# Performance work log

Measured on AMD Instinct MI355X. Metric: run time of the kernel, lower is better.

Reference implementation:

```python
import jax, jax.numpy as jnp
import numpy as np


def setup_inputs() -> dict:
    key = jax.random.key(0)
    ks = jax.random.split(key, 10)
    B, T, E = 4096, 200, 64
    H0, H1, H2 = 80, 40, 1
    D = 4 * E  # concat feature dim = 256
    glorot = lambda k, shp: jax.random.normal(k, shp, jnp.float32) * jnp.sqrt(2.0 / (shp[0] + shp[1]))
    return {
        "queries": jax.random.normal(ks[0], (B, 1, E), jnp.float32),
        "keys": jax.random.normal(ks[1], (B, T, E), jnp.float32),
        "keys_length": jax.random.randint(ks[2], (B, 1), 0, T, jnp.int32),
        "W0": glorot(ks[3], (D, H0)),
        "b0": jnp.zeros((H0,), jnp.float32),
        "W1": glorot(ks[4], (H0, H1)),
        "b1": jnp.zeros((H1,), jnp.float32),
        "W2": glorot(ks[5], (H1, H2)),
        "b2": jnp.zeros((H2,), jnp.float32),
    }


def reference(queries, keys, keys_length, W0, b0, W1, b1, W2, b2):
    B, T, E = keys.shape
    # repeat query along history axis: [B,1,E] -> [B,T,E]
    q = jnp.broadcast_to(queries, (B, T, E))
    # DIN attention input: [B,T,4E]
    att = jnp.concatenate([q, keys, q - keys, q * keys], axis=-1)
    # tiny 3-layer MLP, sigmoid activations (att_activation, no output_activation override)
    h = jax.nn.sigmoid(att @ W0 + b0)
    h = jax.nn.sigmoid(h @ W1 + b1)
    score = jax.nn.sigmoid(h @ W2 + b2)          # [B,T,1]
    out = jnp.transpose(score, (0, 2, 1))         # [B,1,T]
    # sequence mask: [B,1,T]
    key_masks = jnp.arange(T)[None, None, :] < keys_length[:, :, None]
    # weight_normalization=False -> masked positions become 0, no softmax
    out = jnp.where(key_masks, out, jnp.zeros_like(out))
    # weighted sum over history: [B,1,T] @ [B,T,E] -> [B,1,E]
    return jnp.matmul(out, keys)
```

## Files before the change

### kernel.cpp

```cpp
#include <hip/hip_runtime.h>

#define NT 512
#define NWAVE 8
#define PE 136
#define PW1 88
#define PH 88
#define UPB 7
#define BPC 64
#define SPC (BPC * UPB)

typedef __attribute__((ext_vector_type(8))) short short8;
typedef __attribute__((ext_vector_type(4))) float f32x4;

__device__ __forceinline__ unsigned short f2b(float f) {
  unsigned int x = __float_as_uint(f);
  return (unsigned short)((x + 0x7fffu + ((x >> 16) & 1u)) >> 16);
}
__device__ __forceinline__ float sigmoidf(float x) {
  return __builtin_amdgcn_rcpf(1.0f + __expf(-x));
}
__device__ __forceinline__ short8 pack8(float4 a, float4 b) {
  short8 r;
  r[0] = (short)f2b(a.x); r[1] = (short)f2b(a.y); r[2] = (short)f2b(a.z); r[3] = (short)f2b(a.w);
  r[4] = (short)f2b(b.x); r[5] = (short)f2b(b.y); r[6] = (short)f2b(b.z); r[7] = (short)f2b(b.w);
  return r;
}
__device__ __forceinline__ short8 pack8q(float4 a, float4 b, float4 qa, float4 qb) {
  short8 r;
  r[0] = (short)f2b(a.x * qa.x); r[1] = (short)f2b(a.y * qa.y);
  r[2] = (short)f2b(a.z * qa.z); r[3] = (short)f2b(a.w * qa.w);
  r[4] = (short)f2b(b.x * qb.x); r[5] = (short)f2b(b.y * qb.y);
  r[6] = (short)f2b(b.z * qb.z); r[7] = (short)f2b(b.w * qb.w);
  return r;
}

__global__ __launch_bounds__(256, 2) void prep_c(
    const float* __restrict__ q, const float* __restrict__ W0,
    const float* __restrict__ b0, float* __restrict__ C, int B)
{
  __shared__ float Wac[64 * 80];
  __shared__ float qlds[32 * 64];
  const int bbase = blockIdx.x * 32, tid = threadIdx.x;
  for (int idx = tid; idx < 5120; idx += 256) {
    const int e = idx / 80, h = idx - e * 80;
    Wac[idx] = W0[e * 80 + h] + W0[(128 + e) * 80 + h];
  }
  for (int idx = tid; idx < 2048; idx += 256) {
    const int bl = idx >> 6, e = idx & 63;
    const int bg = bbase + bl;
    qlds[idx] = (bg < B) ? q[bg * 64 + e] : 0.0f;
  }
  __syncthreads();
  #pragma unroll
  for (int i = 0; i < 10; ++i) {
    const int idx = tid + i * 256;
    const int bl = idx / 80, h = idx - bl * 80;
    const int bg = bbase + bl;
    if (bg < B) {
      float acc = b0[h];
      #pragma unroll 8
      for (int e = 0; e < 64; ++e) acc += qlds[bl * 64 + e] * Wac[e * 80 + h];
      C[bg * 80 + h] = acc;
    }
  }
}

__global__ __launch_bounds__(NT, 2) void din_attn_main(
    const float* __restrict__ q,
    const float* __restrict__ keys,
    const int* __restrict__ klen,
    const float* __restrict__ W0,
    const float* __restrict__ b0,
    const float* __restrict__ W1,
    const float* __restrict__ b1,
    const float* __restrict__ W2,
    const float* __restrict__ b2,
    float* __restrict__ out,
    const float* __restrict__ Cpre,
    unsigned int* __restrict__ ctrs,
    int B)
{
  __shared__ __align__(16) unsigned short WxT[80 * PE];
  __shared__ __align__(16) unsigned short W1T[48 * PW1];
  __shared__ __align__(16) unsigned short h0s[NWAVE][32 * PH];
  __shared__ __align__(16) float scb[NWAVE][32];

  const int tid = threadIdx.x;

  for (int idx = tid; idx < 128 * 80; idx += NT) {
    const int e = idx / 80, h = idx - e * 80;
    const float v = (e < 64)
        ? (W0[(64 + e) * 80 + h] - W0[(128 + e) * 80 + h])
        : W0[(128 + e) * 80 + h];
    WxT[h * PE + e] = f2b(v);
  }
  for (int idx = tid; idx < 48 * PW1; idx += NT) {
    const int j = idx / PW1, h = idx - j * PW1;
    W1T[idx] = (j < 40 && h < 80) ? f2b(W1[h * 40 + j]) : (unsigned short)0;
  }
  __syncthreads();

  const int wv = __builtin_amdgcn_readfirstlane(tid >> 6);
  const int lane = tid & 63;
  const int lm = lane & 15;
  const int quad = lane >> 4;
  const int gw = blockIdx.x * NWAVE + wv;
  unsigned short* h0 = h0s[wv];
  float* scl = scb[wv];

  float b1v[3], w2v[3];
  #pragma unroll
  for (int nt = 0; nt < 3; ++nt) {
    const int col = nt * 16 + lm;
    b1v[nt] = (col < 40) ? b1[col] : 0.0f;
    w2v[nt] = (col < 40) ? W2[col] : 0.0f;
  }
  const float b2v = b2[0];
  const short8 z8 = {0, 0, 0, 0, 0, 0, 0, 0};
  const float4 z4 = {0.0f, 0.0f, 0.0f, 0.0f};

  auto unit = [&](int b, int u, int L) {
    const float4* q4 = (const float4*)(q + (size_t)b * 64);
    const float4 q0 = q4[quad * 2],     q1 = q4[quad * 2 + 1];
    const float4 q2 = q4[8 + quad * 2], q3 = q4[8 + quad * 2 + 1];

    float cfv[5];
    if (Cpre != nullptr) {
      #pragma unroll
      for (int nt = 0; nt < 5; ++nt) cfv[nt] = Cpre[b * 80 + nt * 16 + lm];
    } else {
      #pragma unroll
      for (int nt = 0; nt < 5; ++nt) cfv[nt] = b0[nt * 16 + lm];
      for (int e = 0; e < 64; ++e) {
        const float qv = q[(size_t)b * 64 + e];
        #pragma unroll
        for (int nt = 0; nt < 5; ++nt)
          cfv[nt] += qv * (W0[e * 80 + nt * 16 + lm] + W0[(128 + e) * 80 + nt * 16 + lm]);
      }
    }

    const float* kb = keys + (size_t)b * 12800;
    const int t0 = u << 5;
    const int nr = min(32, L - t0);
    const bool two = nr > 16;

    short8 a0, a1, aq0, aq1;
    {
      const int t = t0 + lm;
      float4 k0 = z4, k1 = z4, k2 = z4, k3 = z4;
      if (t < L) {
        const float4* kp = (const float4*)(kb + (size_t)t * 64);
        k0 = kp[quad * 2]; k1 = kp[quad * 2 + 1];
        k2 = kp[8 + quad * 2]; k3 = kp[8 + quad * 2 + 1];
      }
      a0 = pack8(k0, k1); a1 = pack8(k2, k3);
      aq0 = pack8q(k0, k1, q0, q1); aq1 = pack8q(k2, k3, q2, q3);
    }
    short8 c0 = z8, c1 = z8, cq0 = z8, cq1 = z8;
    if (two) {
      const int t = t0 + 16 + lm;
      float4 k0 = z4, k1 = z4, k2 = z4, k3 = z4;
      if (t < L) {
        const float4* kp = (const float4*)(kb + (size_t)t * 64);
        k0 = kp[quad * 2]; k1 = kp[quad * 2 + 1];
        k2 = kp[8 + quad * 2]; k3 = kp[8 + quad * 2 + 1];
      }
      c0 = pack8(k0, k1); c1 = pack8(k2, k3);
      cq0 = pack8q(k0, k1, q0, q1); cq1 = pack8q(k2, k3, q2, q3);
    }

    #pragma unroll
    for (int nt = 0; nt < 5; ++nt) {
      const int col = nt * 16 + lm;
      const unsigned short* wr = &WxT[col * PE + quad * 8];
      const short8 w0 = *(const short8*)(wr);
      const short8 w1 = *(const short8*)(wr + 32);
      const short8 w2 = *(const short8*)(wr + 64);
      const short8 w3 = *(const short8*)(wr + 96);
      f32x4 acc;
      acc[0] = cfv[nt]; acc[1] = cfv[nt]; acc[2] = cfv[nt]; acc[3] = cfv[nt];
      acc = __builtin_amdgcn_mfma_f32_16x16x32_bf16(a0,  w0, acc, 0, 0, 0);
      acc = __builtin_amdgcn_mfma_f32_16x16x32_bf16(a1,  w1, acc, 0, 0, 0);
      acc = __builtin_amdgcn_mfma_f32_16x16x32_bf16(aq0, w2, acc, 0, 0, 0);
      acc = __builtin_amdgcn_mfma_f32_16x16x32_bf16(aq1, w3, acc, 0, 0, 0);
      #pragma unroll
      for (int r = 0; r < 4; ++r)
        h0[(quad * 4 + r) * PH + col] = f2b(sigmoidf(acc[r]));
      if (two) {
        f32x4 ac2;
        ac2[0] = cfv[nt]; ac2[1] = cfv[nt]; ac2[2] = cfv[nt]; ac2[3] = cfv[nt];
        ac2 = __builtin_amdgcn_mfma_f32_16x16x32_bf16(c0,  w0, ac2, 0, 0, 0);
        ac2 = __builtin_amdgcn_mfma_f32_16x16x32_bf16(c1,  w1, ac2, 0, 0, 0);
        ac2 = __builtin_amdgcn_mfma_f32_16x16x32_bf16(cq0, w2, ac2, 0, 0, 0);
        ac2 = __builtin_amdgcn_mfma_f32_16x16x32_bf16(cq1, w3, ac2, 0, 0, 0);
        #pragma unroll
        for (int r = 0; r < 4; ++r)
          h0[(16 + quad * 4 + r) * PH + col] = f2b(sigmoidf(ac2[r]));
      }
    }

    const short8 ha00 = *(const short8*)&h0[lm * PH + quad * 8];
    const short8 ha01 = *(const short8*)&h0[lm * PH + 32 + quad * 8];
    short8 ha02 = z8;
    if (quad < 2) ha02 = *(const short8*)&h0[lm * PH + 64 + quad * 8];
    short8 ha10 = z8, ha11 = z8, ha12 = z8;
    if (two) {
      ha10 = *(const short8*)&h0[(16 + lm) * PH + quad * 8];
      ha11 = *(const short8*)&h0[(16 + lm) * PH + 32 + quad * 8];
      if (quad < 2) ha12 = *(const short8*)&h0[(16 + lm) * PH + 64 + quad * 8];
    }
    float pd0[4] = {0, 0, 0, 0}, pd1[4] = {0, 0, 0, 0};
    #pragma unroll
    for (int nt = 0; nt < 3; ++nt) {
      const int col = nt * 16 + lm;
      const unsigned short* wr = &W1T[col * PW1 + quad * 8];
      const short8 wb0 = *(const short8*)(wr);
      const short8 wb1 = *(const short8*)(wr + 32);
      short8 wb2 = z8;
      if (quad < 2) wb2 = *(const short8*)(wr + 64);
      f32x4 acc;
      acc[0] = b1v[nt]; acc[1] = b1v[nt]; acc[2] = b1v[nt]; acc[3] = b1v[nt];
      acc = __builtin_amdgcn_mfma_f32_16x16x32_bf16(ha00, wb0, acc, 0, 0, 0);
      acc = __builtin_amdgcn_mfma_f32_16x16x32_bf16(ha01, wb1, acc, 0, 0, 0);
      acc = __builtin_amdgcn_mfma_f32_16x16x32_bf16(ha02, wb2, acc, 0, 0, 0);
      #pragma unroll
      for (int r = 0; r < 4; ++r) pd0[r] += sigmoidf(acc[r]) * w2v[nt];
      if (two) {
        f32x4 ac2;
        ac2[0] = b1v[nt]; ac2[1] = b1v[nt]; ac2[2] = b1v[nt]; ac2[3] = b1v[nt];
        ac2 = __builtin_amdgcn_mfma_f32_16x16x32_bf16(ha10, wb0, ac2, 0, 0, 0);
        ac2 = __builtin_amdgcn_mfma_f32_16x16x32_bf16(ha11, wb1, ac2, 0, 0, 0);
        ac2 = __builtin_amdgcn_mfma_f32_16x16x32_bf16(ha12, wb2, ac2, 0, 0, 0);
        #pragma unroll
        for (int r = 0; r < 4; ++r) pd1[r] += sigmoidf(ac2[r]) * w2v[nt];
      }
    }
    #pragma unroll
    for (int r = 0; r < 4; ++r) {
      pd0[r] += __shfl_xor(pd0[r], 1);
      pd0[r] += __shfl_xor(pd0[r], 2);
      pd0[r] += __shfl_xor(pd0[r], 4);
      pd0[r] += __shfl_xor(pd0[r], 8);
    }
    if (two) {
      #pragma unroll
      for (int r = 0; r < 4; ++r) {
        pd1[r] += __shfl_xor(pd1[r], 1);
        pd1[r] += __shfl_xor(pd1[r], 2);
        pd1[r] += __shfl_xor(pd1[r], 4);
        pd1[r] += __shfl_xor(pd1[r], 8);
      }
    }
    if (lm == 0) {
      #pragma unroll
      for (int r = 0; r < 4; ++r) scl[quad * 4 + r] = sigmoidf(pd0[r] + b2v);
      if (two) {
        #pragma unroll
        for (int r = 0; r < 4; ++r) scl[16 + quad * 4 + r] = sigmoidf(pd1[r] + b2v);
      }
    }
    float4 sv[8];
    #pragma unroll
    for (int i = 0; i < 8; ++i) sv[i] = *(const float4*)&scl[i * 4];

    const float* kcol = kb + (size_t)t0 * 64 + lane;
    float wacc = 0.0f;
    #pragma unroll
    for (int t = 0; t < 32; ++t) {
      if (t < nr) {
        const int i = t >> 2, j = t & 3;
        const float s = (j == 0) ? sv[i].x : (j == 1) ? sv[i].y : (j == 2) ? sv[i].z : sv[i].w;
        wacc += s * kcol[(size_t)t * 64];
      }
    }
    atomicAdd(&out[(size_t)b * 64 + lane], wacc);
  };

  if (ctrs != nullptr) {
    const int c = gw >> 6;
    unsigned int* ctr = ctrs + (size_t)c * 32;
    unsigned int v0 = 0u;
    if (lane == 0) v0 = atomicAdd(ctr, 1u);
    int s = (int)__builtin_amdgcn_readfirstlane(v0);
    while (s < SPC) {
      unsigned int vn = 0u;
      if (lane == 0) vn = atomicAdd(ctr, 1u);
      const int b = (c << 6) + (s & 63);
      const int u = s >> 6;
      if (b < B) {
        int L = klen[b];
        L = __builtin_amdgcn_readfirstlane(max(0, min(200, L)));
        if (u * 32 < L) unit(b, u, L);
      }
      s = (int)__builtin_amdgcn_readfirstlane(vn);
    }
  } else {
    const int b = gw;
    if (b < B) {
      int L = klen[b];
      L = __builtin_amdgcn_readfirstlane(max(0, min(200, L)));
      for (int u = 0; u * 32 < L; ++u) unit(b, u, L);
    }
  }
}

extern "C" void kernel_launch(void* const* d_in, const int* in_sizes, int n_in,
                              void* d_out, int out_size, void* d_ws, size_t ws_size,
                              hipStream_t stream) {
  const int B = in_sizes[2];
  const size_t csize = (size_t)B * 80 * sizeof(float);
  const int nctr = (B + BPC - 1) / BPC;
  const size_t ctrbytes = (size_t)nctr * 32 * sizeof(unsigned int);

  const float* Cpre = nullptr;
  unsigned int* ctrs = nullptr;
  size_t off = 0;
  if (ws_size >= csize) { Cpre = (const float*)d_ws; off = csize; }
  off = (off + 127) & ~(size_t)127;
  if (ws_size >= off + ctrbytes) {
    ctrs = (unsigned int*)((char*)d_ws + off);
    hipMemsetAsync(ctrs, 0, ctrbytes, stream);
  }
  hipMemsetAsync(d_out, 0, (size_t)out_size, stream);

  if (Cpre != nullptr) {
    prep_c<<<(B + 31) / 32, 256, 0, stream>>>(
        (const float*)d_in[0], (const float*)d_in[3], (const float*)d_in[4],
        (float*)d_ws, B);
  }
  din_attn_main<<<(B + NWAVE - 1) / NWAVE, NT, 0, stream>>>(
      (const float*)d_in[0], (const float*)d_in[1], (const int*)d_in[2],
      (const float*)d_in[3], (const float*)d_in[4], (const float*)d_in[5],
      (const float*)d_in[6], (const float*)d_in[7], (const float*)d_in[8],
      (float*)d_out, Cpre, ctrs, B);
}
```

Before: 370.7 us.

## Build compact work list, software-prefetch next unit, and vectorize weighted-sum reduction

A new pre-kernel builds a compact global list of only the valid (batch, chunk) units, so the main kernel no longer pops masked-out slots from per-cluster counters. The main loop is restructured to prefetch the next unit's keys, klen and C values while computing the current one, hiding global latency. The final weighted sum now uses float4 loads with cross-quad shuffles and fewer atomics instead of going through shared memory. This costs an extra kernel launch, global atomics while building the list, and higher register pressure from the prefetch state.

```diff
diff --git a/kernel.cpp b/kernel.cpp
--- a/kernel.cpp
+++ b/kernel.cpp
@@ -6,8 +6,6 @@
 #define PW1 88
 #define PH 88
 #define UPB 7
-#define BPC 64
-#define SPC (BPC * UPB)
 
 typedef __attribute__((ext_vector_type(8))) short short8;
 typedef __attribute__((ext_vector_type(4))) float f32x4;
@@ -61,6 +59,21 @@
       #pragma unroll 8
       for (int e = 0; e < 64; ++e) acc += qlds[bl * 64 + e] * Wac[e * 80 + h];
       C[bg * 80 + h] = acc;
+    }
+  }
+}
+
+__global__ void build_wl(const int* __restrict__ klen, unsigned* __restrict__ hdr,
+                         unsigned* __restrict__ wl, int B)
+{
+  const int b = blockIdx.x * 256 + threadIdx.x;
+  if (b < B) {
+    int L = klen[b];
+    L = max(0, min(200, L));
+    const int nu = (L + 31) >> 5;
+    for (int u = 0; u < nu; ++u) {
+      const unsigned pos = atomicAdd(&hdr[0], 1u);
+      wl[pos] = ((unsigned)u << 16) | (unsigned)b;
     }
   }
 }
@@ -77,13 +90,13 @@
     const float* __restrict__ b2,
     float* __restrict__ out,
     const float* __restrict__ Cpre,
-    unsigned int* __restrict__ ctrs,
+    unsigned* __restrict__ hdr,
+    const unsigned* __restrict__ wl,
     int B)
 {
   __shared__ __align__(16) unsigned short WxT[80 * PE];
   __shared__ __align__(16) unsigned short W1T[48 * PW1];
   __shared__ __align__(16) unsigned short h0s[NWAVE][32 * PH];
-  __shared__ __align__(16) float scb[NWAVE][32];
 
   const int tid = threadIdx.x;
 
@@ -106,7 +119,8 @@
   const int quad = lane >> 4;
   const int gw = blockIdx.x * NWAVE + wv;
   unsigned short* h0 = h0s[wv];
-  float* scl = scb[wv];
+  const bool dyn = (hdr != nullptr);
+  unsigned* pop = dyn ? (hdr + 32) : nullptr;
 
   float b1v[3], w2v[3];
   #pragma unroll
@@ -117,68 +131,106 @@
   }
   const float b2v = b2[0];
   const short8 z8 = {0, 0, 0, 0, 0, 0, 0, 0};
-  const float4 z4 = {0.0f, 0.0f, 0.0f, 0.0f};
-
-  auto unit = [&](int b, int u, int L) {
-    const float4* q4 = (const float4*)(q + (size_t)b * 64);
-    const float4 q0 = q4[quad * 2],     q1 = q4[quad * 2 + 1];
-    const float4 q2 = q4[8 + quad * 2], q3 = q4[8 + quad * 2 + 1];
-
-    float cfv[5];
+
+  auto pf = [&](int s, int& pb, int& pu, int& pL,
+                float4& K0, float4& K1, float4& K2, float4& K3,
+                float& C0, float& C1, float& C2, float& C3, float& C4) {
+    int b, u;
+    if (dyn) { const unsigned e = wl[s]; b = (int)(e & 0xFFFFu); u = (int)(e >> 16); }
+    else     { b = gw; u = s - gw * UPB; }
+    pb = b; pu = u;
+    pL = klen[b];
     if (Cpre != nullptr) {
-      #pragma unroll
-      for (int nt = 0; nt < 5; ++nt) cfv[nt] = Cpre[b * 80 + nt * 16 + lm];
+      const float* cp = Cpre + (size_t)b * 80 + lm;
+      C0 = cp[0]; C1 = cp[16]; C2 = cp[32]; C3 = cp[48]; C4 = cp[64];
     } else {
-      #pragma unroll
-      for (int nt = 0; nt < 5; ++nt) cfv[nt] = b0[nt * 16 + lm];
+      C0 = b0[lm]; C1 = b0[16 + lm]; C2 = b0[32 + lm]; C3 = b0[48 + lm]; C4 = b0[64 + lm];
       for (int e = 0; e < 64; ++e) {
         const float qv = q[(size_t)b * 64 + e];
-        #pragma unroll
-        for (int nt = 0; nt < 5; ++nt)
-          cfv[nt] += qv * (W0[e * 80 + nt * 16 + lm] + W0[(128 + e) * 80 + nt * 16 + lm]);
-      }
-    }
-
-    const float* kb = keys + (size_t)b * 12800;
-    const int t0 = u << 5;
-    const int nr = min(32, L - t0);
-    const bool two = nr > 16;
-
-    short8 a0, a1, aq0, aq1;
-    {
-      const int t = t0 + lm;
-      float4 k0 = z4, k1 = z4, k2 = z4, k3 = z4;
-      if (t < L) {
-        const float4* kp = (const float4*)(kb + (size_t)t * 64);
-        k0 = kp[quad * 2]; k1 = kp[quad * 2 + 1];
-        k2 = kp[8 + quad * 2]; k3 = kp[8 + quad * 2 + 1];
-      }
-      a0 = pack8(k0, k1); a1 = pack8(k2, k3);
-      aq0 = pack8q(k0, k1, q0, q1); aq1 = pack8q(k2, k3, q2, q3);
-    }
+        C0 += qv * (W0[e * 80 + lm] + W0[(128 + e) * 80 + lm]);
+        C1 += qv * (W0[e * 80 + 16 + lm] + W0[(128 + e) * 80 + 16 + lm]);
+        C2 += qv * (W0[e * 80 + 32 + lm] + W0[(128 + e) * 80 + 32 + lm]);
+        C3 += qv * (W0[e * 80 + 48 + lm] + W0[(128 + e) * 80 + 48 + lm]);
+        C4 += qv * (W0[e * 80 + 64 + lm] + W0[(128 + e) * 80 + 64 + lm]);
+      }
+    }
+    const int t = min(u * 32 + lm, 199);
+    const float4* kp = (const float4*)(keys + (size_t)b * 12800 + (size_t)t * 64);
+    K0 = kp[quad * 2]; K1 = kp[quad * 2 + 1];
+    K2 = kp[8 + quad * 2]; K3 = kp[8 + quad * 2 + 1];
+  };
+
+  int s, nwl;
+  if (dyn) {
+    unsigned v0 = 0u;
+    if (lane == 0) v0 = atomicAdd(pop, 1u);
+    s = (int)__builtin_amdgcn_readfirstlane((int)v0);
+    nwl = (int)__builtin_amdgcn_readfirstlane((int)hdr[0]);
+  } else {
+    s = gw * UPB;
+    nwl = (gw < B) ? (gw * UPB + UPB) : s;
+  }
+
+  int cb = 0, cu = 0, cL = 0;
+  float4 ck0, ck1, ck2, ck3;
+  float cc0 = 0, cc1 = 0, cc2 = 0, cc3 = 0, cc4 = 0;
+  if (s < nwl) pf(s, cb, cu, cL, ck0, ck1, ck2, ck3, cc0, cc1, cc2, cc3, cc4);
+  unsigned vp = 0u;
+  if (dyn && lane == 0) vp = atomicAdd(pop, 1u);
+
+  while (s < nwl) {
+    const float4* q4p = (const float4*)(q + (size_t)cb * 64);
+    const float4 q0 = q4p[quad * 2], q1 = q4p[quad * 2 + 1];
+    const float4 q2v = q4p[8 + quad * 2], q3v = q4p[8 + quad * 2 + 1];
+
+    const int Ls = max(0, min(200, __builtin_amdgcn_readfirstlane(cL)));
+    const int t0 = cu << 5;
+
+    const bool v0ok = (t0 + lm) < Ls;
+    short8 a0 = pack8(ck0, ck1), a1 = pack8(ck2, ck3);
+    short8 aq0 = pack8q(ck0, ck1, q0, q1), aq1 = pack8q(ck2, ck3, q2v, q3v);
+    if (!v0ok) { a0 = z8; a1 = z8; aq0 = z8; aq1 = z8; }
+
+    int s2;
+    if (dyn) {
+      s2 = (int)__builtin_amdgcn_readfirstlane((int)vp);
+      if (lane == 0) vp = atomicAdd(pop, 1u);
+    } else {
+      s2 = s + 1;
+    }
+
+    const bool twoS = (Ls - t0) > 16;
+    float4 e0, e1, e2, e3;
+    if (twoS) {
+      const int t1 = min(t0 + 16 + lm, 199);
+      const float4* kp = (const float4*)(keys + (size_t)cb * 12800 + (size_t)t1 * 64);
+      e0 = kp[quad * 2]; e1 = kp[quad * 2 + 1];
+      e2 = kp[8 + quad * 2]; e3 = kp[8 + quad * 2 + 1];
+    }
+    int nb = 0, nu_ = 0, nL = 0;
+    float4 nk0, nk1, nk2, nk3;
+    float nc0 = 0, nc1 = 0, nc2 = 0, nc3 = 0, nc4 = 0;
+    if (s2 < nwl) pf(s2, nb, nu_, nL, nk0, nk1, nk2, nk3, nc0, nc1, nc2, nc3, nc4);
+
     short8 c0 = z8, c1 = z8, cq0 = z8, cq1 = z8;
-    if (two) {
-      const int t = t0 + 16 + lm;
-      float4 k0 = z4, k1 = z4, k2 = z4, k3 = z4;
-      if (t < L) {
-        const float4* kp = (const float4*)(kb + (size_t)t * 64);
-        k0 = kp[quad * 2]; k1 = kp[quad * 2 + 1];
-        k2 = kp[8 + quad * 2]; k3 = kp[8 + quad * 2 + 1];
-      }
-      c0 = pack8(k0, k1); c1 = pack8(k2, k3);
-      cq0 = pack8q(k0, k1, q0, q1); cq1 = pack8q(k2, k3, q2, q3);
+    if (twoS) {
+      const bool v1ok = (t0 + 16 + lm) < Ls;
+      c0 = pack8(e0, e1); c1 = pack8(e2, e3);
+      cq0 = pack8q(e0, e1, q0, q1); cq1 = pack8q(e2, e3, q2v, q3v);
+      if (!v1ok) { c0 = z8; c1 = z8; cq0 = z8; cq1 = z8; }
     }
 
     #pragma unroll
     for (int nt = 0; nt < 5; ++nt) {
       const int col = nt * 16 + lm;
+      const float cv = (nt == 0) ? cc0 : (nt == 1) ? cc1 : (nt == 2) ? cc2 : (nt == 3) ? cc3 : cc4;
       const unsigned short* wr = &WxT[col * PE + quad * 8];
       const short8 w0 = *(const short8*)(wr);
       const short8 w1 = *(const short8*)(wr + 32);
       const short8 w2 = *(const short8*)(wr + 64);
       const short8 w3 = *(const short8*)(wr + 96);
       f32x4 acc;
-      acc[0] = cfv[nt]; acc[1] = cfv[nt]; acc[2] = cfv[nt]; acc[3] = cfv[nt];
+      acc[0] = cv; acc[1] = cv; acc[2] = cv; acc[3] = cv;
       acc = __builtin_amdgcn_mfma_f32_16x16x32_bf16(a0,  w0, acc, 0, 0, 0);
       acc = __builtin_amdgcn_mfma_f32_16x16x32_bf16(a1,  w1, acc, 0, 0, 0);
       acc = __builtin_amdgcn_mfma_f32_16x16x32_bf16(aq0, w2, acc, 0, 0, 0);
@@ -186,9 +238,9 @@
       #pragma unroll
       for (int r = 0; r < 4; ++r)
         h0[(quad * 4 + r) * PH + col] = f2b(sigmoidf(acc[r]));
-      if (two) {
+      if (twoS) {
         f32x4 ac2;
-        ac2[0] = cfv[nt]; ac2[1] = cfv[nt]; ac2[2] = cfv[nt]; ac2[3] = cfv[nt];
+        ac2[0] = cv; ac2[1] = cv; ac2[2] = cv; ac2[3] = cv;
         ac2 = __builtin_amdgcn_mfma_f32_16x16x32_bf16(c0,  w0, ac2, 0, 0, 0);
         ac2 = __builtin_amdgcn_mfma_f32_16x16x32_bf16(c1,  w1, ac2, 0, 0, 0);
         ac2 = __builtin_amdgcn_mfma_f32_16x16x32_bf16(cq0, w2, ac2, 0, 0, 0);
@@ -204,7 +256,7 @@
     short8 ha02 = z8;
     if (quad < 2) ha02 = *(const short8*)&h0[lm * PH + 64 + quad * 8];
     short8 ha10 = z8, ha11 = z8, ha12 = z8;
-    if (two) {
+    if (twoS) {
       ha10 = *(const short8*)&h0[(16 + lm) * PH + quad * 8];
       ha11 = *(const short8*)&h0[(16 + lm) * PH + 32 + quad * 8];
       if (quad < 2) ha12 = *(const short8*)&h0[(16 + lm) * PH + 64 + quad * 8];
@@ -225,7 +277,7 @@
       acc = __builtin_amdgcn_mfma_f32_16x16x32_bf16(ha02, wb2, acc, 0, 0, 0);
       #pragma unroll
       for (int r = 0; r < 4; ++r) pd0[r] += sigmoidf(acc[r]) * w2v[nt];
-      if (two) {
+      if (twoS) {
         f32x4 ac2;
         ac2[0] = b1v[nt]; ac2[1] = b1v[nt]; ac2[2] = b1v[nt]; ac2[3] = b1v[nt];
         ac2 = __builtin_amdgcn_mfma_f32_16x16x32_bf16(ha10, wb0, ac2, 0, 0, 0);
@@ -242,7 +294,7 @@
       pd0[r] += __shfl_xor(pd0[r], 4);
       pd0[r] += __shfl_xor(pd0[r], 8);
     }
-    if (two) {
+    if (twoS) {
       #pragma unroll
       for (int r = 0; r < 4; ++r) {
         pd1[r] += __shfl_xor(pd1[r], 1);
@@ -251,56 +303,42 @@
         pd1[r] += __shfl_xor(pd1[r], 8);
       }
     }
-    if (lm == 0) {
-      #pragma unroll
-      for (int r = 0; r < 4; ++r) scl[quad * 4 + r] = sigmoidf(pd0[r] + b2v);
-      if (two) {
-        #pragma unroll
-        for (int r = 0; r < 4; ++r) scl[16 + quad * 4 + r] = sigmoidf(pd1[r] + b2v);
-      }
-    }
-    float4 sv[8];
-    #pragma unroll
-    for (int i = 0; i < 8; ++i) sv[i] = *(const float4*)&scl[i * 4];
-
-    const float* kcol = kb + (size_t)t0 * 64 + lane;
-    float wacc = 0.0f;
-    #pragma unroll
-    for (int t = 0; t < 32; ++t) {
-      if (t < nr) {
-        const int i = t >> 2, j = t & 3;
-        const float s = (j == 0) ? sv[i].x : (j == 1) ? sv[i].y : (j == 2) ? sv[i].z : sv[i].w;
-        wacc += s * kcol[(size_t)t * 64];
-      }
-    }
-    atomicAdd(&out[(size_t)b * 64 + lane], wacc);
-  };
-
-  if (ctrs != nullptr) {
-    const int c = gw >> 6;
-    unsigned int* ctr = ctrs + (size_t)c * 32;
-    unsigned int v0 = 0u;
-    if (lane == 0) v0 = atomicAdd(ctr, 1u);
-    int s = (int)__builtin_amdgcn_readfirstlane(v0);
-    while (s < SPC) {
-      unsigned int vn = 0u;
-      if (lane == 0) vn = atomicAdd(ctr, 1u);
-      const int b = (c << 6) + (s & 63);
-      const int u = s >> 6;
-      if (b < B) {
-        int L = klen[b];
-        L = __builtin_amdgcn_readfirstlane(max(0, min(200, L)));
-        if (u * 32 < L) unit(b, u, L);
-      }
-      s = (int)__builtin_amdgcn_readfirstlane(vn);
-    }
-  } else {
-    const int b = gw;
-    if (b < B) {
-      int L = klen[b];
-      L = __builtin_amdgcn_readfirstlane(max(0, min(200, L)));
-      for (int u = 0; u * 32 < L; ++u) unit(b, u, L);
-    }
+    float sc0[4], sc1[4];
+    #pragma unroll
+    for (int r = 0; r < 4; ++r) {
+      const int ta = t0 + 4 * quad + r;
+      sc0[r] = (ta < Ls) ? sigmoidf(pd0[r] + b2v) : 0.0f;
+      sc1[r] = (twoS && (ta + 16) < Ls) ? sigmoidf(pd1[r] + b2v) : 0.0f;
+    }
+
+    const float* kb = keys + (size_t)cb * 12800;
+    float4 w4 = {0.0f, 0.0f, 0.0f, 0.0f};
+    #pragma unroll
+    for (int r = 0; r < 4; ++r) {
+      const int ta = t0 + 4 * quad + r;
+      const float4 kva = *(const float4*)(kb + (size_t)min(ta, 199) * 64 + 4 * lm);
+      w4.x += sc0[r] * kva.x; w4.y += sc0[r] * kva.y;
+      w4.z += sc0[r] * kva.z; w4.w += sc0[r] * kva.w;
+      if (twoS) {
+        const float4 kvb = *(const float4*)(kb + (size_t)min(ta + 16, 199) * 64 + 4 * lm);
+        w4.x += sc1[r] * kvb.x; w4.y += sc1[r] * kvb.y;
+        w4.z += sc1[r] * kvb.z; w4.w += sc1[r] * kvb.w;
+      }
+    }
+    w4.x += __shfl_xor(w4.x, 16); w4.y += __shfl_xor(w4.y, 16);
+    w4.z += __shfl_xor(w4.z, 16); w4.w += __shfl_xor(w4.w, 16);
+    w4.x += __shfl_xor(w4.x, 32); w4.y += __shfl_xor(w4.y, 32);
+    w4.z += __shfl_xor(w4.z, 32); w4.w += __shfl_xor(w4.w, 32);
+    if (lane < 16) {
+      float* op = out + (size_t)cb * 64 + 4 * lm;
+      atomicAdd(op + 0, w4.x); atomicAdd(op + 1, w4.y);
+      atomicAdd(op + 2, w4.z); atomicAdd(op + 3, w4.w);
+    }
+
+    cb = nb; cu = nu_; cL = nL;
+    ck0 = nk0; ck1 = nk1; ck2 = nk2; ck3 = nk3;
+    cc0 = nc0; cc1 = nc1; cc2 = nc2; cc3 = nc3; cc4 = nc4;
+    s = s2;
   }
 }
 
@@ -309,20 +347,25 @@
                               hipStream_t stream) {
   const int B = in_sizes[2];
   const size_t csize = (size_t)B * 80 * sizeof(float);
-  const int nctr = (B + BPC - 1) / BPC;
-  const size_t ctrbytes = (size_t)nctr * 32 * sizeof(unsigned int);
+  const size_t wlbytes = (size_t)B * UPB * sizeof(unsigned);
 
   const float* Cpre = nullptr;
-  unsigned int* ctrs = nullptr;
+  unsigned* hdr = nullptr;
+  unsigned* wl = nullptr;
   size_t off = 0;
   if (ws_size >= csize) { Cpre = (const float*)d_ws; off = csize; }
   off = (off + 127) & ~(size_t)127;
-  if (ws_size >= off + ctrbytes) {
-    ctrs = (unsigned int*)((char*)d_ws + off);
-    hipMemsetAsync(ctrs, 0, ctrbytes, stream);
+  if (ws_size >= off + 256 + wlbytes) {
+    hdr = (unsigned*)((char*)d_ws + off);
+    wl = hdr + 64;
+    hipMemsetAsync(hdr, 0, 256, stream);
   }
   hipMemsetAsync(d_out, 0, (size_t)out_size, stream);
 
+  if (hdr != nullptr) {
+    build_wl<<<(B + 255) / 256, 256, 0, stream>>>(
+        (const int*)d_in[2], hdr, wl, B);
+  }
   if (Cpre != nullptr) {
     prep_c<<<(B + 31) / 32, 256, 0, stream>>>(
         (const float*)d_in[0], (const float*)d_in[3], (const float*)d_in[4],
@@ -332,5 +375,5 @@
       (const float*)d_in[0], (const float*)d_in[1], (const int*)d_in[2],
       (const float*)d_in[3], (const float*)d_in[4], (const float*)d_in[5],
       (const float*)d_in[6], (const float*)d_in[7], (const float*)d_in[8],
-      (float*)d_out, Cpre, ctrs, B);
-}
+      (float*)d_out, Cpre, hdr, (const unsigned*)wl, B);
+}
```

Result: slower. 544.2 us (+46.8%).

## Replace atomic work-stealing with one-wave-per-batch loop and prefetched keys

Applied to the files above, without the earlier changes.

Drops the per-chunk atomic counter scheduler and the atomicAdd accumulation. Each wave now owns one batch row and loops over its 32-step chunks, prefetching the next chunk's keys while computing the current one. The weighted sum is kept in registers and reduced with shuffles into a single float4 store, which also removes both memsets. It adds s_setprio around the MFMA sections. The trade-off is the loss of dynamic load balancing: keys_length varies from 0 to 199, so waves with long rows become stragglers.

```diff
diff --git a/kernel.cpp b/kernel.cpp
--- a/kernel.cpp
+++ b/kernel.cpp
@@ -5,9 +5,6 @@
 #define PE 136
 #define PW1 88
 #define PH 88
-#define UPB 7
-#define BPC 64
-#define SPC (BPC * UPB)
 
 typedef __attribute__((ext_vector_type(8))) short short8;
 typedef __attribute__((ext_vector_type(4))) float f32x4;
@@ -77,13 +74,11 @@
     const float* __restrict__ b2,
     float* __restrict__ out,
     const float* __restrict__ Cpre,
-    unsigned int* __restrict__ ctrs,
     int B)
 {
   __shared__ __align__(16) unsigned short WxT[80 * PE];
   __shared__ __align__(16) unsigned short W1T[48 * PW1];
   __shared__ __align__(16) unsigned short h0s[NWAVE][32 * PH];
-  __shared__ __align__(16) float scb[NWAVE][32];
 
   const int tid = threadIdx.x;
 
@@ -104,25 +99,18 @@
   const int lane = tid & 63;
   const int lm = lane & 15;
   const int quad = lane >> 4;
-  const int gw = blockIdx.x * NWAVE + wv;
+  const int b = blockIdx.x * NWAVE + wv;
   unsigned short* h0 = h0s[wv];
-  float* scl = scb[wv];
-
-  float b1v[3], w2v[3];
-  #pragma unroll
-  for (int nt = 0; nt < 3; ++nt) {
-    const int col = nt * 16 + lm;
-    b1v[nt] = (col < 40) ? b1[col] : 0.0f;
-    w2v[nt] = (col < 40) ? W2[col] : 0.0f;
-  }
-  const float b2v = b2[0];
   const short8 z8 = {0, 0, 0, 0, 0, 0, 0, 0};
-  const float4 z4 = {0.0f, 0.0f, 0.0f, 0.0f};
-
-  auto unit = [&](int b, int u, int L) {
-    const float4* q4 = (const float4*)(q + (size_t)b * 64);
-    const float4 q0 = q4[quad * 2],     q1 = q4[quad * 2 + 1];
-    const float4 q2 = q4[8 + quad * 2], q3 = q4[8 + quad * 2 + 1];
+
+  if (b < B) {
+    int L = klen[b];
+    L = __builtin_amdgcn_readfirstlane(max(0, min(200, L)));
+    const int nu = (L + 31) >> 5;
+
+    const float4* q4p = (const float4*)(q + (size_t)b * 64);
+    const float4 q0 = q4p[quad * 2], q1 = q4p[quad * 2 + 1];
+    const float4 q2 = q4p[8 + quad * 2], q3 = q4p[8 + quad * 2 + 1];
 
     float cfv[5];
     if (Cpre != nullptr) {
@@ -138,169 +126,167 @@
           cfv[nt] += qv * (W0[e * 80 + nt * 16 + lm] + W0[(128 + e) * 80 + nt * 16 + lm]);
       }
     }
-
-    const float* kb = keys + (size_t)b * 12800;
-    const int t0 = u << 5;
-    const int nr = min(32, L - t0);
-    const bool two = nr > 16;
-
-    short8 a0, a1, aq0, aq1;
-    {
-      const int t = t0 + lm;
-      float4 k0 = z4, k1 = z4, k2 = z4, k3 = z4;
-      if (t < L) {
-        const float4* kp = (const float4*)(kb + (size_t)t * 64);
-        k0 = kp[quad * 2]; k1 = kp[quad * 2 + 1];
-        k2 = kp[8 + quad * 2]; k3 = kp[8 + quad * 2 + 1];
-      }
-      a0 = pack8(k0, k1); a1 = pack8(k2, k3);
-      aq0 = pack8q(k0, k1, q0, q1); aq1 = pack8q(k2, k3, q2, q3);
-    }
-    short8 c0 = z8, c1 = z8, cq0 = z8, cq1 = z8;
-    if (two) {
-      const int t = t0 + 16 + lm;
-      float4 k0 = z4, k1 = z4, k2 = z4, k3 = z4;
-      if (t < L) {
-        const float4* kp = (const float4*)(kb + (size_t)t * 64);
-        k0 = kp[quad * 2]; k1 = kp[quad * 2 + 1];
-        k2 = kp[8 + quad * 2]; k3 = kp[8 + quad * 2 + 1];
-      }
-      c0 = pack8(k0, k1); c1 = pack8(k2, k3);
-      cq0 = pack8q(k0, k1, q0, q1); cq1 = pack8q(k2, k3, q2, q3);
-    }
-
-    #pragma unroll
-    for (int nt = 0; nt < 5; ++nt) {
-      const int col = nt * 16 + lm;
-      const unsigned short* wr = &WxT[col * PE + quad * 8];
-      const short8 w0 = *(const short8*)(wr);
-      const short8 w1 = *(const short8*)(wr + 32);
-      const short8 w2 = *(const short8*)(wr + 64);
-      const short8 w3 = *(const short8*)(wr + 96);
-      f32x4 acc;
-      acc[0] = cfv[nt]; acc[1] = cfv[nt]; acc[2] = cfv[nt]; acc[3] = cfv[nt];
-      acc = __builtin_amdgcn_mfma_f32_16x16x32_bf16(a0,  w0, acc, 0, 0, 0);
-      acc = __builtin_amdgcn_mfma_f32_16x16x32_bf16(a1,  w1, acc, 0, 0, 0);
-      acc = __builtin_amdgcn_mfma_f32_16x16x32_bf16(aq0, w2, acc, 0, 0, 0);
-      acc = __builtin_amdgcn_mfma_f32_16x16x32_bf16(aq1, w3, acc, 0, 0, 0);
-      #pragma unroll
-      for (int r = 0; r < 4; ++r)
-        h0[(quad * 4 + r) * PH + col] = f2b(sigmoidf(acc[r]));
-      if (two) {
-        f32x4 ac2;
-        ac2[0] = cfv[nt]; ac2[1] = cfv[nt]; ac2[2] = cfv[nt]; ac2[3] = cfv[nt];
-        ac2 = __builtin_amdgcn_mfma_f32_16x16x32_bf16(c0,  w0, ac2, 0, 0, 0);
-        ac2 = __builtin_amdgcn_mfma_f32_16x16x32_bf16(c1,  w1, ac2, 0, 0, 0);
-        ac2 = __builtin_amdgcn_mfma_f32_16x16x32_bf16(cq0, w2, ac2, 0, 0, 0);
-        ac2 = __builtin_amdgcn_mfma_f32_16x16x32_bf16(cq1, w3, ac2, 0, 0, 0);
-        #pragma unroll
-        for (int r = 0; r < 4; ++r)
-          h0[(16 + quad * 4 + r) * PH + col] = f2b(sigmoidf(ac2[r]));
-      }
-    }
-
-    const short8 ha00 = *(const short8*)&h0[lm * PH + quad * 8];
-    const short8 ha01 = *(const short8*)&h0[lm * PH + 32 + quad * 8];
-    short8 ha02 = z8;
-    if (quad < 2) ha02 = *(const short8*)&h0[lm * PH + 64 + quad * 8];
-    short8 ha10 = z8, ha11 = z8, ha12 = z8;
-    if (two) {
-      ha10 = *(const short8*)&h0[(16 + lm) * PH + quad * 8];
-      ha11 = *(const short8*)&h0[(16 + lm) * PH + 32 + quad * 8];
-      if (quad < 2) ha12 = *(const short8*)&h0[(16 + lm) * PH + 64 + quad * 8];
-    }
-    float pd0[4] = {0, 0, 0, 0}, pd1[4] = {0, 0, 0, 0};
+    float b1v[3], w2v[3];
     #pragma unroll
     for (int nt = 0; nt < 3; ++nt) {
       const int col = nt * 16 + lm;
-      const unsigned short* wr = &W1T[col * PW1 + quad * 8];
-      const short8 wb0 = *(const short8*)(wr);
-      const short8 wb1 = *(const short8*)(wr + 32);
-      short8 wb2 = z8;
-      if (quad < 2) wb2 = *(const short8*)(wr + 64);
-      f32x4 acc;
-      acc[0] = b1v[nt]; acc[1] = b1v[nt]; acc[2] = b1v[nt]; acc[3] = b1v[nt];
-      acc = __builtin_amdgcn_mfma_f32_16x16x32_bf16(ha00, wb0, acc, 0, 0, 0);
-      acc = __builtin_amdgcn_mfma_f32_16x16x32_bf16(ha01, wb1, acc, 0, 0, 0);
-      acc = __builtin_amdgcn_mfma_f32_16x16x32_bf16(ha02, wb2, acc, 0, 0, 0);
-      #pragma unroll
-      for (int r = 0; r < 4; ++r) pd0[r] += sigmoidf(acc[r]) * w2v[nt];
-      if (two) {
-        f32x4 ac2;
-        ac2[0] = b1v[nt]; ac2[1] = b1v[nt]; ac2[2] = b1v[nt]; ac2[3] = b1v[nt];
-        ac2 = __builtin_amdgcn_mfma_f32_16x16x32_bf16(ha10, wb0, ac2, 0, 0, 0);
-        ac2 = __builtin_amdgcn_mfma_f32_16x16x32_bf16(ha11, wb1, ac2, 0, 0, 0);
-        ac2 = __builtin_amdgcn_mfma_f32_16x16x32_bf16(ha12, wb2, ac2, 0, 0, 0);
+      b1v[nt] = (col < 40) ? b1[col] : 0.0f;
+      w2v[nt] = (col < 40) ? W2[col] : 0.0f;
+    }
+    const float b2v = b2[0];
+
+    const float* kb = keys + (size_t)b * 12800;
+    float4 w4 = {0.0f, 0.0f, 0.0f, 0.0f};
+
+    float4 pk0, pk1, pk2, pk3;
+    if (nu > 0) {
+      const float4* kp = (const float4*)(kb + (size_t)min(lm, 199) * 64);
+      pk0 = kp[quad * 2]; pk1 = kp[quad * 2 + 1];
+      pk2 = kp[8 + quad * 2]; pk3 = kp[8 + quad * 2 + 1];
+    }
+
+    for (int u = 0; u < nu; ++u) {
+      const int t0 = u << 5;
+      const bool twoS = (L - t0) > 16;
+
+      short8 a0 = pack8(pk0, pk1), a1 = pack8(pk2, pk3);
+      short8 aq0 = pack8q(pk0, pk1, q0, q1), aq1 = pack8q(pk2, pk3, q2, q3);
+      if (!((t0 + lm) < L)) { a0 = z8; a1 = z8; aq0 = z8; aq1 = z8; }
+
+      float4 e0, e1, e2, e3;
+      if (twoS) {
+        const float4* kp = (const float4*)(kb + (size_t)min(t0 + 16 + lm, 199) * 64);
+        e0 = kp[quad * 2]; e1 = kp[quad * 2 + 1];
+        e2 = kp[8 + quad * 2]; e3 = kp[8 + quad * 2 + 1];
+      }
+      if (u + 1 < nu) {
+        const float4* kp = (const float4*)(kb + (size_t)min(t0 + 32 + lm, 199) * 64);
+        pk0 = kp[quad * 2]; pk1 = kp[quad * 2 + 1];
+        pk2 = kp[8 + quad * 2]; pk3 = kp[8 + quad * 2 + 1];
+      }
+
+      short8 c0 = z8, c1 = z8, cq0 = z8, cq1 = z8;
+      if (twoS) {
+        c0 = pack8(e0, e1); c1 = pack8(e2, e3);
+        cq0 = pack8q(e0, e1, q0, q1); cq1 = pack8q(e2, e3, q2, q3);
+        if (!((t0 + 16 + lm) < L)) { c0 = z8; c1 = z8; cq0 = z8; cq1 = z8; }
+      }
+
+      __builtin_amdgcn_s_setprio(1);
+      #pragma unroll
+      for (int nt = 0; nt < 5; ++nt) {
+        const int col = nt * 16 + lm;
+        const unsigned short* wr = &WxT[col * PE + quad * 8];
+        const short8 w0 = *(const short8*)(wr);
+        const short8 w1 = *(const short8*)(wr + 32);
+        const short8 w2 = *(const short8*)(wr + 64);
+        const short8 w3 = *(const short8*)(wr + 96);
+        f32x4 acc;
+        acc[0] = cfv[nt]; acc[1] = cfv[nt]; acc[2] = cfv[nt]; acc[3] = cfv[nt];
+        acc = __builtin_amdgcn_mfma_f32_16x16x32_bf16(a0,  w0, acc, 0, 0, 0);
+        acc = __builtin_amdgcn_mfma_f32_16x16x32_bf16(a1,  w1, acc, 0, 0, 0);
+        acc = __builtin_amdgcn_mfma_f32_16x16x32_bf16(aq0, w2, acc, 0, 0, 0);
+        acc = __builtin_amdgcn_mfma_f32_16x16x32_bf16(aq1, w3, acc, 0, 0, 0);
         #pragma unroll
-        for (int r = 0; r < 4; ++r) pd1[r] += sigmoidf(ac2[r]) * w2v[nt];
-      }
-    }
-    #pragma unroll
-    for (int r = 0; r < 4; ++r) {
-      pd0[r] += __shfl_xor(pd0[r], 1);
-      pd0[r] += __shfl_xor(pd0[r], 2);
-      pd0[r] += __shfl_xor(pd0[r], 4);
-      pd0[r] += __shfl_xor(pd0[r], 8);
-    }
-    if (two) {
+        for (int r = 0; r < 4; ++r)
+          h0[(quad * 4 + r) * PH + col] = f2b(sigmoidf(acc[r]));
+        if (twoS) {
+          f32x4 ac2;
+          ac2[0] = cfv[nt]; ac2[1] = cfv[nt]; ac2[2] = cfv[nt]; ac2[3] = cfv[nt];
+          ac2 = __builtin_amdgcn_mfma_f32_16x16x32_bf16(c0,  w0, ac2, 0, 0, 0);
+          ac2 = __builtin_amdgcn_mfma_f32_16x16x32_bf16(c1,  w1, ac2, 0, 0, 0);
+          ac2 = __builtin_amdgcn_mfma_f32_16x16x32_bf16(cq0, w2, ac2, 0, 0, 0);
+          ac2 = __builtin_amdgcn_mfma_f32_16x16x32_bf16(cq1, w3, ac2, 0, 0, 0);
+          #pragma unroll
+          for (int r = 0; r < 4; ++r)
+            h0[(16 + quad * 4 + r) * PH + col] = f2b(sigmoidf(ac2[r]));
+        }
+      }
+      __builtin_amdgcn_s_setprio(0);
+
+      const short8 ha00 = *(const short8*)&h0[lm * PH + quad * 8];
+      const short8 ha01 = *(const short8*)&h0[lm * PH + 32 + quad * 8];
+      short8 ha02 = z8;
+      if (quad < 2) ha02 = *(const short8*)&h0[lm * PH + 64 + quad * 8];
+      short8 ha10 = z8, ha11 = z8, ha12 = z8;
+      if (twoS) {
+        ha10 = *(const short8*)&h0[(16 + lm) * PH + quad * 8];
+        ha11 = *(const short8*)&h0[(16 + lm) * PH + 32 + quad * 8];
+        if (quad < 2) ha12 = *(const short8*)&h0[(16 + lm) * PH + 64 + quad * 8];
+      }
+      float pd0[4] = {0, 0, 0, 0}, pd1[4] = {0, 0, 0, 0};
+      __builtin_amdgcn_s_setprio(1);
+      #pragma unroll
+      for (int nt = 0; nt < 3; ++nt) {
+        const int col = nt * 16 + lm;
+        const unsigned short* wr = &W1T[col * PW1 + quad * 8];
+        const short8 wb0 = *(const short8*)(wr);
+        const short8 wb1 = *(const short8*)(wr + 32);
+        short8 wb2 = z8;
+        if (quad < 2) wb2 = *(const short8*)(wr + 64);
+        f32x4 acc;
+        acc[0] = b1v[nt]; acc[1] = b1v[nt]; acc[2] = b1v[nt]; acc[3] = b1v[nt];
+        acc = __builtin_amdgcn_mfma_f32_16x16x32_bf16(ha00, wb0, acc, 0, 0, 0);
+        acc = __builtin_amdgcn_mfma_f32_16x16x32_bf16(ha01, wb1, acc, 0, 0, 0);
+        acc = __builtin_amdgcn_mfma_f32_16x16x32_bf16(ha02, wb2, acc, 0, 0, 0);
+        #pragma unroll
+        for (int r = 0; r < 4; ++r) pd0[r] += sigmoidf(acc[r]) * w2v[nt];
+        if (twoS) {
+          f32x4 ac2;
+          ac2[0] = b1v[nt]; ac2[1] = b1v[nt]; ac2[2] = b1v[nt]; ac2[3] = b1v[nt];
+          ac2 = __builtin_amdgcn_mfma_f32_16x16x32_bf16(ha10, wb0, ac2, 0, 0, 0);
+          ac2 = __builtin_amdgcn_mfma_f32_16x16x32_bf16(ha11, wb1, ac2, 0, 0, 0);
+          ac2 = __builtin_amdgcn_mfma_f32_16x16x32_bf16(ha12, wb2, ac2, 0, 0, 0);
+          #pragma unroll
+          for (int r = 0; r < 4; ++r) pd1[r] += sigmoidf(ac2[r]) * w2v[nt];
+        }
+      }
+      __builtin_amdgcn_s_setprio(0);
+
       #pragma unroll
       for (int r = 0; r < 4; ++r) {
-        pd1[r] += __shfl_xor(pd1[r], 1);
-        pd1[r] += __shfl_xor(pd1[r], 2);
-        pd1[r] += __shfl_xor(pd1[r], 4);
-        pd1[r] += __shfl_xor(pd1[r], 8);
-      }
-    }
-    if (lm == 0) {
-      #pragma unroll
-      for (int r = 0; r < 4; ++r) scl[quad * 4 + r] = sigmoidf(pd0[r] + b2v);
-      if (two) {
+        pd0[r] += __shfl_xor(pd0[r], 1);
+        pd0[r] += __shfl_xor(pd0[r], 2);
+        pd0[r] += __shfl_xor(pd0[r], 4);
+        pd0[r] += __shfl_xor(pd0[r], 8);
+      }
+      if (twoS) {
         #pragma unroll
-        for (int r = 0; r < 4; ++r) scl[16 + quad * 4 + r] = sigmoidf(pd1[r] + b2v);
-      }
-    }
-    float4 sv[8];
-    #pragma unroll
-    for (int i = 0; i < 8; ++i) sv[i] = *(const float4*)&scl[i * 4];
-
-    const float* kcol = kb + (size_t)t0 * 64 + lane;
-    float wacc = 0.0f;
-    #pragma unroll
-    for (int t = 0; t < 32; ++t) {
-      if (t < nr) {
-        const int i = t >> 2, j = t & 3;
-        const float s = (j == 0) ? sv[i].x : (j == 1) ? sv[i].y : (j == 2) ? sv[i].z : sv[i].w;
-        wacc += s * kcol[(size_t)t * 64];
-      }
-    }
-    atomicAdd(&out[(size_t)b * 64 + lane], wacc);
-  };
-
-  if (ctrs != nullptr) {
-    const int c = gw >> 6;
-    unsigned int* ctr = ctrs + (size_t)c * 32;
-    unsigned int v0 = 0u;
-    if (lane == 0) v0 = atomicAdd(ctr, 1u);
-    int s = (int)__builtin_amdgcn_readfirstlane(v0);
-    while (s < SPC) {
-      unsigned int vn = 0u;
-      if (lane == 0) vn = atomicAdd(ctr, 1u);
-      const int b = (c << 6) + (s & 63);
-      const int u = s >> 6;
-      if (b < B) {
-        int L = klen[b];
-        L = __builtin_amdgcn_readfirstlane(max(0, min(200, L)));
-        if (u * 32 < L) unit(b, u, L);
-      }
-      s = (int)__builtin_amdgcn_readfirstlane(vn);
-    }
-  } else {
-    const int b = gw;
-    if (b < B) {
-      int L = klen[b];
-      L = __builtin_amdgcn_readfirstlane(max(0, min(200, L)));
-      for (int u = 0; u * 32 < L; ++u) unit(b, u, L);
-    }
+        for (int r = 0; r < 4; ++r) {
+          pd1[r] += __shfl_xor(pd1[r], 1);
+          pd1[r] += __shfl_xor(pd1[r], 2);
+          pd1[r] += __shfl_xor(pd1[r], 4);
+          pd1[r] += __shfl_xor(pd1[r], 8);
+        }
+      }
+      float sc0[4], sc1[4];
+      #pragma unroll
+      for (int r = 0; r < 4; ++r) {
+        const int ta = t0 + 4 * quad + r;
+        sc0[r] = (ta < L) ? sigmoidf(pd0[r] + b2v) : 0.0f;
+        sc1[r] = (twoS && (ta + 16) < L) ? sigmoidf(pd1[r] + b2v) : 0.0f;
+      }
+
+      #pragma unroll
+      for (int r = 0; r < 4; ++r) {
+        const int ta = t0 + 4 * quad + r;
+        const float4 kva = *(const float4*)(kb + (size_t)min(ta, 199) * 64 + 4 * lm);
+        w4.x += sc0[r] * kva.x; w4.y += sc0[r] * kva.y;
+        w4.z += sc0[r] * kva.z; w4.w += sc0[r] * kva.w;
+        if (twoS) {
+          const float4 kvb = *(const float4*)(kb + (size_t)min(ta + 16, 199) * 64 + 4 * lm);
+          w4.x += sc1[r] * kvb.x; w4.y += sc1[r] * kvb.y;
+          w4.z += sc1[r] * kvb.z; w4.w += sc1[r] * kvb.w;
+        }
+      }
+    }
+
+    w4.x += __shfl_xor(w4.x, 16); w4.y += __shfl_xor(w4.y, 16);
+    w4.z += __shfl_xor(w4.z, 16); w4.w += __shfl_xor(w4.w, 16);
+    w4.x += __shfl_xor(w4.x, 32); w4.y += __shfl_xor(w4.y, 32);
+    w4.z += __shfl_xor(w4.z, 32); w4.w += __shfl_xor(w4.w, 32);
+    if (lane < 16)
+      *(float4*)(out + (size_t)b * 64 + 4 * lm) = w4;
   }
 }
 
@@ -308,29 +294,16 @@
                               void* d_out, int out_size, void* d_ws, size_t ws_size,
                               hipStream_t stream) {
   const int B = in_sizes[2];
-  const size_t csize = (size_t)B * 80 * sizeof(float);
-  const int nctr = (B + BPC - 1) / BPC;
-  const size_t ctrbytes = (size_t)nctr * 32 * sizeof(unsigned int);
-
   const float* Cpre = nullptr;
-  unsigned int* ctrs = nullptr;
-  size_t off = 0;
-  if (ws_size >= csize) { Cpre = (const float*)d_ws; off = csize; }
-  off = (off + 127) & ~(size_t)127;
-  if (ws_size >= off + ctrbytes) {
-    ctrs = (unsigned int*)((char*)d_ws + off);
-    hipMemsetAsync(ctrs, 0, ctrbytes, stream);
-  }
-  hipMemsetAsync(d_out, 0, (size_t)out_size, stream);
-
-  if (Cpre != nullptr) {
+  if (ws_size >= (size_t)B * 80 * sizeof(float)) {
+    float* C = (float*)d_ws;
     prep_c<<<(B + 31) / 32, 256, 0, stream>>>(
-        (const float*)d_in[0], (const float*)d_in[3], (const float*)d_in[4],
-        (float*)d_ws, B);
+        (const float*)d_in[0], (const float*)d_in[3], (const float*)d_in[4], C, B);
+    Cpre = C;
   }
   din_attn_main<<<(B + NWAVE - 1) / NWAVE, NT, 0, stream>>>(
       (const float*)d_in[0], (const float*)d_in[1], (const int*)d_in[2],
       (const float*)d_in[3], (const float*)d_in[4], (const float*)d_in[5],
       (const float*)d_in[6], (const float*)d_in[7], (const float*)d_in[8],
-      (float*)d_out, Cpre, ctrs, B);
-}
+      (float*)d_out, Cpre, B);
+}
```

New measurement: 381.9 us. 3.0% more time.
